# Performance work log

Measured on AMD Instinct MI355X. Metric: run time of the kernel, lower is better.

Reference implementation:

```python
import jax, jax.numpy as jnp
import numpy as np

HIDDEN = 1024
NUM_HEADS = 8
HEAD_DIM = HIDDEN // NUM_HEADS
MAX_BACKWARD = 11   # context_left - 1
MAX_FORWARD = 12    # context_right
SPAN = MAX_BACKWARD + MAX_FORWARD + 1  # 24

B, U, W, C = 8, 16, 128, 151


def setup_inputs() -> dict:
    key = jax.random.key(0)
    kq, kk, kp = jax.random.split(key, 3)
    queries = jax.random.normal(kq, (B, U, W, NUM_HEADS, HEAD_DIM), dtype=jnp.float32)
    keys = jax.random.normal(kk, (B, U, C, NUM_HEADS, HEAD_DIM), dtype=jnp.float32)
    # glorot-ish scale for pos_proj (hidden, num_heads*head_dim)
    pos_proj = jax.random.normal(kp, (HIDDEN, NUM_HEADS * HEAD_DIM), dtype=jnp.float32) * (1.0 / np.sqrt(HIDDEN))
    return {"queries": queries, "keys": keys, "pos_proj": pos_proj}


def _sinusoid_emb(pos_proj):
    # positions: max_backward .. -max_forward (descending), shape (SPAN,)
    pos = jnp.arange(MAX_BACKWARD, -(MAX_FORWARD + 1), -1, dtype=jnp.float32)
    num_ts = HIDDEN // 2
    inv_ts = jnp.ones((num_ts,), dtype=jnp.float32)  # module uses ones
    scaled = pos[:, None] * inv_ts[None, :]          # (SPAN, HIDDEN/2)
    signal = jnp.concatenate([jnp.sin(scaled), jnp.cos(scaled)], axis=-1)  # (SPAN, HIDDEN)
    proj = signal @ pos_proj                         # (SPAN, N*H)
    return proj.reshape(SPAN, NUM_HEADS, HEAD_DIM)


def _relative_shift(term_bd, context_size):
    # term_bd: (B, N, U, W, SPAN) -> (B, N, U, W, C)
    b, n, u, w, _ = term_bd.shape
    pad = context_size + 1 - SPAN
    padded = jnp.pad(term_bd, ((0, 0), (0, 0), (0, 0), (0, 0), (0, pad)))
    flat = padded.reshape(b, n, u, w * (context_size + 1))
    sliced = flat[:, :, :, : w * context_size]
    return sliced.reshape(b, n, u, w, context_size)


def reference(queries, keys, pos_proj):
    context_size = keys.shape[2]
    sin_emb = _sinusoid_emb(pos_proj)                      # (SPAN, N, H)
    qp = jnp.transpose(queries, (0, 3, 1, 2, 4))           # (B, N, U, W, H)
    kp = jnp.transpose(keys, (0, 3, 1, 4, 2))              # (B, N, U, H, C)
    term_ac = jnp.matmul(qp, kp)                           # (B, N, U, W, C)
    # term_bd: query-position interaction, (B, N, U, W, SPAN)
    term_bd = jnp.einsum("bnuwh,fnh->bnuwf", qp, sin_emb)
    term_bd = _relative_shift(term_bd, context_size)       # (B, N, U, W, C)
    return term_ac + term_bd
```

## Files before the change

### kernel.cpp

```cpp
#include <hip/hip_runtime.h>
#include <cmath>

#define NHEADS 8
#define HDIM 128
#define SPAN 24
#define U_ 16
#define W_ 128
#define C_ 151
#define HID 1024

typedef unsigned short ushort8v __attribute__((ext_vector_type(8)));
typedef unsigned short ushort4v __attribute__((ext_vector_type(4)));
typedef __bf16 bf16x8 __attribute__((ext_vector_type(8)));
typedef float f32x4 __attribute__((ext_vector_type(4)));

__device__ inline unsigned short f2bf(float f) {
    union { float f; unsigned u; } v; v.f = f;
    unsigned r = v.u + 0x7FFFu + ((v.u >> 16) & 1u);
    return (unsigned short)(r >> 16);
}
__device__ inline float bf2f(unsigned short u) {
    union { unsigned u; float f; } v; v.u = ((unsigned)u) << 16;
    return v.f;
}
__device__ inline ushort8v cvt8(float4 a, float4 b) {
    ushort8v v;
    v[0] = f2bf(a.x); v[1] = f2bf(a.y); v[2] = f2bf(a.z); v[3] = f2bf(a.w);
    v[4] = f2bf(b.x); v[5] = f2bf(b.y); v[6] = f2bf(b.z); v[7] = f2bf(b.w);
    return v;
}

__global__ void k_partial(const float* __restrict__ pp, float* __restrict__ part) {
    const int bi = blockIdx.x >> 2, cj = blockIdx.x & 3;
    const int col = cj * 256 + threadIdx.x * 4;
    const int row0 = bi * 16;
    float4 s = make_float4(0.f, 0.f, 0.f, 0.f);
    #pragma unroll
    for (int i = 0; i < 16; ++i) {
        float4 v = *(const float4*)(pp + (size_t)(row0 + i) * HID + col);
        s.x += v.x; s.y += v.y; s.z += v.z; s.w += v.w;
    }
    *(float4*)(part + (size_t)bi * HID + col) = s;
}

struct SC { float s[SPAN]; float c[SPAN]; };

#define CHUNK_B 8192
#define AUX_OFF 16384
#define S12_OFF (AUX_OFF + 4096)
#define BD_PITCH 25

__device__ inline ushort8v emb8(const char* lds_raw, int f, int u16, const SC& sc) {
    float4 s1a = *(const float4*)(lds_raw + S12_OFF + u16 * 32);
    float4 s1b = *(const float4*)(lds_raw + S12_OFF + u16 * 32 + 16);
    float4 s2a = *(const float4*)(lds_raw + S12_OFF + 512 + u16 * 32);
    float4 s2b = *(const float4*)(lds_raw + S12_OFF + 512 + u16 * 32 + 16);
    const float sf = sc.s[f], cf = sc.c[f];
    ushort8v v;
    v[0] = f2bf(sf * s1a.x + cf * s2a.x); v[1] = f2bf(sf * s1a.y + cf * s2a.y);
    v[2] = f2bf(sf * s1a.z + cf * s2a.z); v[3] = f2bf(sf * s1a.w + cf * s2a.w);
    v[4] = f2bf(sf * s1b.x + cf * s2b.x); v[5] = f2bf(sf * s1b.y + cf * s2b.y);
    v[6] = f2bf(sf * s1b.z + cf * s2b.z); v[7] = f2bf(sf * s1b.w + cf * s2b.w);
    return v;
}

#define ISSUE_K(c, P0, P1)                                                     \
    {                                                                          \
        const int r_ = 32 * (c) + (tid >> 4);                                  \
        if (r_ < C_) {                                                         \
            const float* s_ = k + kbase + (size_t)r_ * HID + u16 * 8;          \
            P0 = *(const float4*)s_; P1 = *(const float4*)(s_ + 4);            \
        }                                                                      \
    }

#define WRITE_PURE(c, P0, P1, BUFOFF)                                          \
    {                                                                          \
        const int rl_ = tid >> 4;                                              \
        const int dst_ = (BUFOFF) + rl_ * 256 + ((u16 * 16) ^ ((rl_ & 7) << 4));\
        *(ushort8v*)(lds_raw + dst_) = cvt8(P0, P1);                           \
    }

#define WRITE_C4(P0, P1, BUFOFF)                                               \
    {                                                                          \
        const int rl_ = tid >> 4;                                              \
        const int r_ = 128 + rl_;                                              \
        const int dst_ = (BUFOFF) + rl_ * 256 + ((u16 * 16) ^ ((rl_ & 7) << 4));\
        ushort8v v_;                                                           \
        if (r_ < C_) v_ = cvt8(P0, P1);                                        \
        else         v_ = emb8(lds_raw, r_ - C_, u16, sc);                     \
        *(ushort8v*)(lds_raw + dst_) = v_;                                     \
    }

#define WRITE_C5(BUFOFF)                                                       \
    if (tid < 256) {                                                           \
        const int rl_ = tid >> 4;                                              \
        const int r_ = 160 + rl_;                                              \
        const int dst_ = (BUFOFF) + rl_ * 256 + ((u16 * 16) ^ ((rl_ & 7) << 4));\
        ushort8v v_;                                                           \
        if (r_ < 175) v_ = emb8(lds_raw, r_ - C_, u16, sc);                    \
        else          v_ = (ushort8v)(unsigned short)0;                        \
        *(ushort8v*)(lds_raw + dst_) = v_;                                     \
    }

#define MFMA2(c, BUFOFF)                                                       \
    {                                                                          \
        _Pragma("unroll")                                                      \
        for (int kk = 0; kk < 4; ++kk) {                                       \
            _Pragma("unroll")                                                  \
            for (int jj = 0; jj < 2; ++jj) {                                   \
                const int rl = jj * 16 + lr;                                   \
                const int byt = (BUFOFF) + rl * 256 +                          \
                                (((kk * 64) + (lk * 16)) ^ ((rl & 7) << 4));   \
                bf16x8 bf = __builtin_bit_cast(bf16x8,                         \
                                *(const ushort8v*)(lds_raw + byt));            \
                acc[2 * (c) + jj] = __builtin_amdgcn_mfma_f32_16x16x32_bf16(   \
                                        qf[kk], bf, acc[2 * (c) + jj], 0, 0, 0);\
            }                                                                  \
        }                                                                      \
    }

#define MFMA1(BUFOFF)                                                          \
    {                                                                          \
        _Pragma("unroll")                                                      \
        for (int kk = 0; kk < 4; ++kk) {                                       \
            const int rl = lr;                                                 \
            const int byt = (BUFOFF) + rl * 256 +                              \
                            (((kk * 64) + (lk * 16)) ^ ((rl & 7) << 4));       \
            bf16x8 bf = __builtin_bit_cast(bf16x8,                             \
                            *(const ushort8v*)(lds_raw + byt));                \
            acc[10] = __builtin_amdgcn_mfma_f32_16x16x32_bf16(                 \
                          qf[kk], bf, acc[10], 0, 0, 0);                       \
        }                                                                      \
    }

__global__ __launch_bounds__(512, 4) void k_main(const float* __restrict__ q,
                                                 const float* __restrict__ k,
                                                 const float* __restrict__ part,
                                                 float* __restrict__ out, SC sc) {
    __shared__ __align__(16) char lds_raw[AUX_OFF + W_ * BD_PITCH * 2];
    unsigned short* bd = (unsigned short*)(lds_raw + AUX_OFF);

    const int bid = blockIdx.x;
    const int n = bid & 7;
    const int u = (bid >> 3) & 15;
    const int b = bid >> 7;

    const size_t qbase = ((size_t)(b * U_ + u) * W_) * HID + n * HDIM;
    const size_t kbase = ((size_t)(b * U_ + u) * C_) * HID + n * HDIM;
    const size_t obase = ((size_t)((b * NHEADS + n) * U_ + u)) * (W_ * C_);

    const int tid = threadIdx.x;
    const int lane = tid & 63;
    const int wave = tid >> 6;
    const int w0 = wave * 16;
    const int lr = lane & 15;
    const int lk = lane >> 4;
    const int u16 = tid & 15;

    const int c4 = tid & 31, rg = tid >> 5;
    float4 pp4[4];
    #pragma unroll
    for (int i = 0; i < 4; ++i)
        pp4[i] = *(const float4*)(part + (size_t)(rg * 4 + i) * HID + n * HDIM + c4 * 4);

    float4 a0, a1, b0, b1;
    ISSUE_K(0, a0, a1);
    ISSUE_K(1, b0, b1);

    const float* qrow = q + qbase + (size_t)(w0 + lr) * HID + lk * 8;
    float4 qpf[8];
    #pragma unroll
    for (int kk = 0; kk < 4; ++kk) {
        qpf[2 * kk]     = *(const float4*)(qrow + kk * 32);
        qpf[2 * kk + 1] = *(const float4*)(qrow + kk * 32 + 4);
    }

    {
        float4 rs;
        rs.x = pp4[0].x + pp4[1].x + pp4[2].x + pp4[3].x;
        rs.y = pp4[0].y + pp4[1].y + pp4[2].y + pp4[3].y;
        rs.z = pp4[0].z + pp4[1].z + pp4[2].z + pp4[3].z;
        rs.w = pp4[0].w + pp4[1].w + pp4[2].w + pp4[3].w;
        ushort4v rb;
        rb[0] = f2bf(rs.x); rb[1] = f2bf(rs.y); rb[2] = f2bf(rs.z); rb[3] = f2bf(rs.w);
        *(ushort4v*)(lds_raw + AUX_OFF + rg * 256 + c4 * 8) = rb;
    }
    WRITE_PURE(0, a0, a1, 0);
    __syncthreads();

    if (tid < 256) {
        const int col = tid & 127, half = tid >> 7;
        float s = 0.f;
        #pragma unroll
        for (int g = 0; g < 8; ++g)
            s += bf2f(*(const unsigned short*)(lds_raw + AUX_OFF + (half * 8 + g) * 256 + col * 2));
        *(float*)(lds_raw + S12_OFF + (half * 128 + col) * 4) = s;
    }
    bf16x8 qf[4];
    #pragma unroll
    for (int kk = 0; kk < 4; ++kk)
        qf[kk] = __builtin_bit_cast(bf16x8, cvt8(qpf[2 * kk], qpf[2 * kk + 1]));

    f32x4 acc[11];
    #pragma unroll
    for (int j = 0; j < 11; ++j) acc[j] = (f32x4)(0.f);

    __syncthreads();

    WRITE_PURE(1, b0, b1, CHUNK_B);  ISSUE_K(2, a0, a1);  MFMA2(0, 0);
    __syncthreads();
    WRITE_PURE(2, a0, a1, 0);        ISSUE_K(3, b0, b1);  MFMA2(1, CHUNK_B);
    __syncthreads();
    WRITE_PURE(3, b0, b1, CHUNK_B);  ISSUE_K(4, a0, a1);  MFMA2(2, 0);
    __syncthreads();
    WRITE_C4(a0, a1, 0);                                  MFMA2(3, CHUNK_B);
    __syncthreads();
    WRITE_C5(CHUNK_B);                                    MFMA2(4, 0);
    __syncthreads();
    MFMA1(CHUNK_B);

    {
        const int c9 = 144 + lr;
        if (c9 >= C_) {
            const int f = c9 - C_;
            #pragma unroll
            for (int reg = 0; reg < 4; ++reg) {
                const int w = w0 + lk * 4 + reg;
                bd[w * BD_PITCH + f] = f2bf(acc[9][reg]);
            }
        }
        const int f10 = 9 + lr;
        if (f10 < SPAN) {
            #pragma unroll
            for (int reg = 0; reg < 4; ++reg) {
                const int w = w0 + lk * 4 + reg;
                bd[w * BD_PITCH + f10] = f2bf(acc[10][reg]);
            }
        }
    }

    #pragma unroll
    for (int j = 0; j < 10; ++j) {
        const int c = j * 16 + lr;
        if (c < C_) {
            #pragma unroll
            for (int reg = 0; reg < 4; ++reg) {
                const int w = w0 + lk * 4 + reg;
                float v = acc[j][reg];
                const int d = c - w;
                if (d >= 0 && d < SPAN) v += bf2f(bd[w * BD_PITCH + d]);
                out[obase + (size_t)w * C_ + c] = v;
            }
        }
    }
}

extern "C" void kernel_launch(void* const* d_in, const int* in_sizes, int n_in,
                              void* d_out, int out_size, void* d_ws, size_t ws_size,
                              hipStream_t stream) {
    const float* queries = (const float*)d_in[0];
    const float* keys    = (const float*)d_in[1];
    const float* posproj = (const float*)d_in[2];
    float* out = (float*)d_out;

    float* part = (float*)d_ws;

    SC sc;
    for (int f = 0; f < SPAN; ++f) {
        float p = (float)(11 - f);
        sc.s[f] = sinf(p);
        sc.c[f] = cosf(p);
    }

    k_partial<<<256, 64, 0, stream>>>(posproj, part);
    k_main<<<1024, 512, 0, stream>>>(queries, keys, part, out, sc);
}
```

Baseline: 50.62 us.

## Reorder K chunk pipeline to process tail chunk first and interleave output stores

Reorders the key-chunk pipeline so the tail chunk (which produces the positional bd terms) is computed first. That lets finished output tiles be written to global memory while later MFMA chunks are still running. It also replaces __syncthreads with a custom lgkmcnt-wait-plus-barrier asm macro. The aim is to overlap the output-store phase with compute and cut barrier overhead. The risk is that the custom barrier does not wait on vector memory and that register pressure rises.

```diff
diff --git a/kernel.cpp b/kernel.cpp
--- a/kernel.cpp
+++ b/kernel.cpp
@@ -29,6 +29,8 @@
     v[4] = f2bf(b.x); v[5] = f2bf(b.y); v[6] = f2bf(b.z); v[7] = f2bf(b.w);
     return v;
 }
+
+#define BAR() asm volatile("s_waitcnt lgkmcnt(0)\n\ts_barrier" ::: "memory")
 
 __global__ void k_partial(const float* __restrict__ pp, float* __restrict__ part) {
     const int bi = blockIdx.x >> 2, cj = blockIdx.x & 3;
@@ -73,7 +75,7 @@
         }                                                                      \
     }
 
-#define WRITE_PURE(c, P0, P1, BUFOFF)                                          \
+#define WRITE_PURE(P0, P1, BUFOFF)                                             \
     {                                                                          \
         const int rl_ = tid >> 4;                                              \
         const int dst_ = (BUFOFF) + rl_ * 256 + ((u16 * 16) ^ ((rl_ & 7) << 4));\
@@ -133,6 +135,21 @@
         }                                                                      \
     }
 
+#define STORE_TILE(J)                                                          \
+    {                                                                          \
+        const int c_ = (J) * 16 + lr;                                          \
+        if (c_ < C_) {                                                         \
+            _Pragma("unroll")                                                  \
+            for (int reg = 0; reg < 4; ++reg) {                                \
+                const int w_ = w0 + lk * 4 + reg;                              \
+                float v_ = acc[J][reg];                                        \
+                const int d_ = c_ - w_;                                        \
+                if (d_ >= 0 && d_ < SPAN) v_ += bf2f(bd[w_ * BD_PITCH + d_]);  \
+                out[obase + (size_t)w_ * C_ + c_] = v_;                        \
+            }                                                                  \
+        }                                                                      \
+    }
+
 __global__ __launch_bounds__(512, 4) void k_main(const float* __restrict__ q,
                                                  const float* __restrict__ k,
                                                  const float* __restrict__ part,
@@ -163,10 +180,6 @@
     for (int i = 0; i < 4; ++i)
         pp4[i] = *(const float4*)(part + (size_t)(rg * 4 + i) * HID + n * HDIM + c4 * 4);
 
-    float4 a0, a1, b0, b1;
-    ISSUE_K(0, a0, a1);
-    ISSUE_K(1, b0, b1);
-
     const float* qrow = q + qbase + (size_t)(w0 + lr) * HID + lk * 8;
     float4 qpf[8];
     #pragma unroll
@@ -174,6 +187,10 @@
         qpf[2 * kk]     = *(const float4*)(qrow + kk * 32);
         qpf[2 * kk + 1] = *(const float4*)(qrow + kk * 32 + 4);
     }
+
+    float4 a0, a1, b0, b1;
+    ISSUE_K(4, a0, a1);
+    ISSUE_K(0, b0, b1);
 
     {
         float4 rs;
@@ -185,8 +202,7 @@
         rb[0] = f2bf(rs.x); rb[1] = f2bf(rs.y); rb[2] = f2bf(rs.z); rb[3] = f2bf(rs.w);
         *(ushort4v*)(lds_raw + AUX_OFF + rg * 256 + c4 * 8) = rb;
     }
-    WRITE_PURE(0, a0, a1, 0);
-    __syncthreads();
+    BAR();
 
     if (tid < 256) {
         const int col = tid & 127, half = tid >> 7;
@@ -205,20 +221,17 @@
     #pragma unroll
     for (int j = 0; j < 11; ++j) acc[j] = (f32x4)(0.f);
 
-    __syncthreads();
-
-    WRITE_PURE(1, b0, b1, CHUNK_B);  ISSUE_K(2, a0, a1);  MFMA2(0, 0);
-    __syncthreads();
-    WRITE_PURE(2, a0, a1, 0);        ISSUE_K(3, b0, b1);  MFMA2(1, CHUNK_B);
-    __syncthreads();
-    WRITE_PURE(3, b0, b1, CHUNK_B);  ISSUE_K(4, a0, a1);  MFMA2(2, 0);
-    __syncthreads();
-    WRITE_C4(a0, a1, 0);                                  MFMA2(3, CHUNK_B);
-    __syncthreads();
-    WRITE_C5(CHUNK_B);                                    MFMA2(4, 0);
-    __syncthreads();
+    BAR();
+
+    WRITE_C4(a0, a1, 0);
+    BAR();
+
+    MFMA2(4, 0);
+    WRITE_C5(CHUNK_B);
+    ISSUE_K(1, a0, a1);
+    BAR();
+
     MFMA1(CHUNK_B);
-
     {
         const int c9 = 144 + lr;
         if (c9 >= C_) {
@@ -238,21 +251,35 @@
             }
         }
     }
-
-    #pragma unroll
-    for (int j = 0; j < 10; ++j) {
-        const int c = j * 16 + lr;
-        if (c < C_) {
-            #pragma unroll
-            for (int reg = 0; reg < 4; ++reg) {
-                const int w = w0 + lk * 4 + reg;
-                float v = acc[j][reg];
-                const int d = c - w;
-                if (d >= 0 && d < SPAN) v += bf2f(bd[w * BD_PITCH + d]);
-                out[obase + (size_t)w * C_ + c] = v;
-            }
-        }
-    }
+    WRITE_PURE(b0, b1, 0);
+    ISSUE_K(2, b0, b1);
+    BAR();
+
+    MFMA2(0, 0);
+    WRITE_PURE(a0, a1, CHUNK_B);
+    ISSUE_K(3, a0, a1);
+    STORE_TILE(8);
+    STORE_TILE(9);
+    BAR();
+
+    MFMA2(1, CHUNK_B);
+    WRITE_PURE(b0, b1, 0);
+    STORE_TILE(0);
+    STORE_TILE(1);
+    BAR();
+
+    MFMA2(2, 0);
+    WRITE_PURE(a0, a1, CHUNK_B);
+    STORE_TILE(2);
+    STORE_TILE(3);
+    BAR();
+
+    MFMA2(3, CHUNK_B);
+    STORE_TILE(4);
+    STORE_TILE(5);
+
+    STORE_TILE(6);
+    STORE_TILE(7);
 }
 
 extern "C" void kernel_launch(void* const* d_in, const int* in_sizes, int n_in,
```

Result: faster. 49.43 us (-2.4%).
